# Optimization experiments

Hardware: AMD Instinct MI355X
Metric: run time of the kernel (lower is better)

## Reference

```python
import jax, jax.numpy as jnp
import numpy as np

H, DH = 16, 64  # n_head, head_dim


def setup_inputs() -> dict:
    key = jax.random.key(0)
    ks = jax.random.split(key, 14)
    B, L, D = 2, 1024, 1024
    d = DH

    def lin_w(k, fan_in, shape):
        return jax.random.normal(k, shape, jnp.float32) / np.sqrt(fan_in)

    return {
        "x": jax.random.normal(ks[0], (B, L, D), jnp.float32),
        "Wq": lin_w(ks[1], D, (D, D)),
        "bq": jnp.zeros((D,), jnp.float32),
        "Wk1": lin_w(ks[2], D, (D, D)),
        "bk1": jnp.zeros((D,), jnp.float32),
        "Wk2": lin_w(ks[3], D, (D, D)),
        "bk2": jnp.zeros((D,), jnp.float32),
        "Wg": lin_w(ks[4], d, (d, 1)),
        "bg": jnp.zeros((1,), jnp.float32),
        "Ws": lin_w(ks[5], d, (d, 1)),
        "bs": jnp.zeros((1,), jnp.float32),
        "Wp": lin_w(ks[6], D, (D, D)),
        "bp": jnp.zeros((D,), jnp.float32),
    }


def reference(x, Wq, bq, Wk1, bk1, Wk2, bk2, Wg, bg, Ws, bs, Wp, bp):
    B, L, D = x.shape
    d = DH
    # AR (GLA) branch
    Q = (x @ Wq + bq).reshape(B, L, H, d)
    K = (x @ Wk1 + bk1).reshape(B, L, H, d)
    V = x.reshape(B, L, H, d)
    W = jnp.einsum('blhd,blhe->blhde', K, V)  # (B,L,H,d,d) outer products
    # stable cumprod of sigmoid gate via log-cumsum-exp trick
    G = jax.nn.sigmoid(x.reshape(B, L, H, d) @ Wg + bg)            # (B,L,H,1)
    log_cum = jnp.clip(jnp.cumsum(jnp.log(jnp.clip(G, 1e-6, None)), axis=1), -30.0, 30.0)
    Gc = (jnp.exp(log_cum) + 1e-6)[..., None]                       # (B,L,H,1,1)
    R = jax.nn.silu(K @ Ws + bs)[..., None]                         # (B,L,H,1,1) decay gate
    Wc = jnp.cumsum(W * R / Gc, axis=1) * Gc                        # weighted cumsum
    O1 = jnp.einsum('blhd,blhde->blhe', Q, Wc)                      # (B,L,H,d)
    # MA branch on one-step residuals
    E = V[:, 1:] - O1[:, :-1]                                       # (B,L-1,H,d)
    q2 = -jax.nn.leaky_relu(-Q[:, :-1] / np.sqrt(d), 0.02)          # ma_q_activation (scale head_dim)
    k2 = jax.nn.sigmoid((x[:, :-1] @ Wk2 + bk2) / np.sqrt(D) * 0.02)  # ma_k_activation (scale n_embd)
    k2 = k2.reshape(B, L - 1, H, d)
    W_ma = jnp.cumsum(jnp.einsum('blhd,blhe->blhde', k2, E), axis=1)
    O2 = jnp.einsum('blhd,blhde->blhe', q2, W_ma)
    O2 = jnp.concatenate([jnp.zeros_like(O2[:, :1]), O2], axis=1)   # shift: first MA output is 0
    O = (O1 + O2).reshape(B, L, D)
    return O @ Wp + bp
```

## Files before the change

kernel.cpp:

```cpp
#include <hip/hip_runtime.h>
#include <hip/hip_bf16.h>
#include <math.h>

#define B_  2
#define L_  1024
#define D_  1024
#define H_  16
#define DH_ 64
#define M_  (B_*L_)
#define CHUNK 64
#define NCH (L_/CHUNK)
#define PT 72
#define PS 76

#define KSCALE (0.02f/32.0f)

using bf16x8 = __attribute__((ext_vector_type(8))) short;
using f32x4  = __attribute__((ext_vector_type(4))) float;

__device__ __forceinline__ unsigned short bf16r(float f){
  union{float f; unsigned int u;} x; x.f = f;
  unsigned int r = x.u + 0x7FFF + ((x.u>>16)&1);
  return (unsigned short)(r>>16);
}
__device__ __forceinline__ float bf2f(unsigned short u){
  union{unsigned int u; float f;} x; x.u = ((unsigned int)u)<<16; return x.f;
}

__global__ __launch_bounds__(256) void f32_to_bf16(
  const float* __restrict__ src, unsigned short* __restrict__ dst, int n4)
{
  int i = blockIdx.x*256 + threadIdx.x;
  int stride = gridDim.x*256;
  for (; i < n4; i += stride){
    float4 v = ((const float4*)src)[i];
    ushort4 o;
    o.x = bf16r(v.x); o.y = bf16r(v.y); o.z = bf16r(v.z); o.w = bf16r(v.w);
    ((ushort4*)dst)[i] = o;
  }
}

__global__ __launch_bounds__(256) void convert_wt(
  const float* __restrict__ W0, const float* __restrict__ W1,
  const float* __restrict__ W2, const float* __restrict__ W3,
  unsigned short* __restrict__ T0, unsigned short* __restrict__ T1,
  unsigned short* __restrict__ T2, unsigned short* __restrict__ T3)
{
  int which = blockIdx.z;
  const float* W = which==0?W0: which==1?W1: which==2?W2: W3;
  unsigned short* T = which==0?T0: which==1?T1: which==2?T2: T3;
  __shared__ float tile[64][65];
  int kBase = blockIdx.x*64, nBase = blockIdx.y*64;
  #pragma unroll
  for (int i=0;i<16;i++){
    int idx = threadIdx.x + i*256;
    int r = idx>>6, c = idx&63;
    tile[r][c] = W[(size_t)(kBase+r)*D_ + nBase+c];
  }
  __syncthreads();
  #pragma unroll
  for (int i=0;i<16;i++){
    int idx = threadIdx.x + i*256;
    int n = idx>>6, k = idx&63;
    T[(size_t)(nBase+n)*D_ + kBase+k] = bf16r(tile[k][n]);
  }
}

__device__ __forceinline__ void gemm_core(
    const unsigned short* __restrict__ A, const unsigned short* __restrict__ Bt,
    const float* __restrict__ bias, float* __restrict__ C,
    unsigned short* __restrict__ Cbf, int epi,
    int rowBase, int colBase)
{
  __shared__ __align__(16) unsigned short As[128*32];
  __shared__ __align__(16) unsigned short Bs[64*32];
  int tid = threadIdx.x, w = tid>>6, l = tid&63;
  int lr = l&15, g4 = l>>4;
  f32x4 acc[2][4];
  #pragma unroll
  for (int mi=0;mi<2;mi++)
    #pragma unroll
    for (int ni=0;ni<4;ni++)
      acc[mi][ni] = (f32x4){0.f,0.f,0.f,0.f};

  for (int k0 = 0; k0 < D_; k0 += 32) {
    #pragma unroll
    for (int i=0;i<2;i++){
      int F = (w*2+i)*64 + l;
      int r = F>>2, c16 = F&3;
      int sc = c16 ^ ((r>>1)&3);
      const unsigned short* g = A + (size_t)(rowBase+r)*D_ + k0 + sc*8;
      __builtin_amdgcn_global_load_lds(
        (const __attribute__((address_space(1))) void*)g,
        (__attribute__((address_space(3))) void*)(As + (size_t)(w*2+i)*512), 16, 0, 0);
    }
    {
      int F = w*64 + l;
      int r = F>>2, c16 = F&3;
      int sc = c16 ^ ((r>>1)&3);
      const unsigned short* g = Bt + (size_t)(colBase+r)*D_ + k0 + sc*8;
      __builtin_amdgcn_global_load_lds(
        (const __attribute__((address_space(1))) void*)g,
        (__attribute__((address_space(3))) void*)(Bs + (size_t)w*512), 16, 0, 0);
    }
    __syncthreads();
    bf16x8 af[2], bfr[4];
    #pragma unroll
    for (int mi=0;mi<2;mi++){
      int row = w*32 + mi*16 + lr;
      af[mi] = *(const bf16x8*)(As + row*32 + ((g4 ^ ((row>>1)&3))*8));
    }
    #pragma unroll
    for (int ni=0;ni<4;ni++){
      int n = ni*16 + lr;
      bfr[ni] = *(const bf16x8*)(Bs + n*32 + ((g4 ^ ((n>>1)&3))*8));
    }
    #pragma unroll
    for (int mi=0;mi<2;mi++)
      #pragma unroll
      for (int ni=0;ni<4;ni++)
        acc[mi][ni] = __builtin_amdgcn_mfma_f32_16x16x32_bf16(af[mi], bfr[ni], acc[mi][ni], 0,0,0);
    __syncthreads();
  }

  #pragma unroll
  for (int mi=0;mi<2;mi++){
    #pragma unroll
    for (int ni=0;ni<4;ni++){
      int col = colBase + ni*16 + lr;
      float bv = bias[col];
      #pragma unroll
      for (int r=0;r<4;r++){
        int row = rowBase + w*32 + mi*16 + g4*4 + r;
        float v = acc[mi][ni][r] + bv;
        if (epi) v = 1.f/(1.f + expf(-v*KSCALE));
        C[(size_t)row*D_ + col] = v;
        if (Cbf) Cbf[(size_t)row*D_ + col] = bf16r(v);
      }
    }
  }
}

__global__ __launch_bounds__(256) void gemm3(
  const unsigned short* __restrict__ A,
  const unsigned short* __restrict__ T0, const unsigned short* __restrict__ T1,
  const unsigned short* __restrict__ T2,
  const float* __restrict__ b0, const float* __restrict__ b1, const float* __restrict__ b2,
  float* __restrict__ C0, float* __restrict__ C1, float* __restrict__ C2,
  unsigned short* __restrict__ F0, unsigned short* __restrict__ F1,
  unsigned short* __restrict__ F2)
{
  int z = blockIdx.z;
  const unsigned short* Bt = z==0?T0: z==1?T1: T2;
  const float* bias = z==0?b0: z==1?b1: b2;
  float* C = z==0?C0: z==1?C1: C2;
  unsigned short* F = z==0?F0: z==1?F1: F2;
  gemm_core(A, Bt, bias, C, F, z==2 ? 1 : 0, blockIdx.x*128, blockIdx.y*64);
}

__global__ __launch_bounds__(256) void gemm1(
  const unsigned short* __restrict__ A, const unsigned short* __restrict__ Bt,
  const float* __restrict__ bias, float* __restrict__ C)
{
  gemm_core(A, Bt, bias, C, nullptr, 0, blockIdx.x*128, blockIdx.y*64);
}

__global__ __launch_bounds__(256) void scalars_kernel(
  const float* __restrict__ X, const float* __restrict__ K,
  const float* __restrict__ Wg, const float* __restrict__ bg,
  const float* __restrict__ Ws, const float* __restrict__ bs,
  float* __restrict__ GL, float* __restrict__ RR)
{
  int item = blockIdx.x * 4 + (threadIdx.x >> 6);
  int ln = threadIdx.x & 63;
  int row = item >> 4;
  int h = item & 15;
  float xv = X[(size_t)row*D_ + h*64 + ln];
  float kv = K[(size_t)row*D_ + h*64 + ln];
  float gdot = xv * Wg[ln];
  float rdot = kv * Ws[ln];
  #pragma unroll
  for (int off = 32; off; off >>= 1) {
    gdot += __shfl_xor(gdot, off);
    rdot += __shfl_xor(rdot, off);
  }
  if (ln == 0) {
    float glogit = gdot + bg[0];
    float sg = 1.f/(1.f+expf(-glogit));
    sg = fmaxf(sg, 1e-6f);
    GL[item] = logf(sg);
    float rlogit = rdot + bs[0];
    RR[item] = rlogit / (1.f + expf(-rlogit));
  }
}

__global__ __launch_bounds__(256) void gl_scan(
  const float* __restrict__ GL, const float* __restrict__ RR,
  float* __restrict__ GC, float* __restrict__ CF)
{
  int bh = blockIdx.x * 4 + (threadIdx.x >> 6);
  int b = bh >> 4, h = bh & 15;
  int ln = threadIdx.x & 63;
  float carry = 0.f;
  for (int it = 0; it < 16; ++it) {
    int l = it*64 + ln;
    float x = GL[((size_t)(b*L_ + l))*H_ + h];
    #pragma unroll
    for (int off = 1; off < 64; off <<= 1) {
      float t = __shfl_up(x, off);
      if (ln >= off) x += t;
    }
    float tot = __shfl(x, 63);
    float cum = carry + x;
    carry += tot;
    float lc = fminf(fmaxf(cum, -30.f), 30.f);
    float gc = expf(lc) + 1e-6f;
    GC[(size_t)bh*L_ + l] = gc;
    CF[(size_t)bh*L_ + l] = RR[((size_t)(b*L_ + l))*H_ + h] / gc;
  }
}

__global__ __launch_bounds__(256) void ar_chunk_sum(
  const unsigned short* __restrict__ Kbf, const unsigned short* __restrict__ Xbf,
  const float* __restrict__ CF, float* __restrict__ CS)
{
  int bh = blockIdx.x, c = blockIdx.y;
  int b = bh >> 4, h = bh & 15;
  int row0 = b*L_ + c*CHUNK;
  __shared__ __align__(16) unsigned short kt_t[64*PT];
  __shared__ __align__(16) unsigned short cv_t[64*PT];
  __shared__ __align__(16) float uni[64*PS];
  __shared__ float cf_s[64];
  int tid = threadIdx.x;
  if (tid < 64) cf_s[tid] = CF[(size_t)bh*L_ + c*CHUNK + tid];
  __syncthreads();
  const unsigned short* kg = Kbf + (size_t)row0*D_ + h*64;
  const unsigned short* vg = Xbf + (size_t)row0*D_ + h*64;
  #pragma unroll
  for (int t=0;t<16;t++){
    int idx = tid + t*256;
    int j = idx>>6, d = idx&63;
    kt_t[d*PT + j] = kg[(size_t)j*D_ + d];
    cv_t[d*PT + j] = bf16r(bf2f(vg[(size_t)j*D_ + d]) * cf_s[j]);
  }
  __syncthreads();
  int w = tid>>6, l = tid&63, lr = l&15, g4 = l>>4;
  f32x4 acc[4];
  #pragma unroll
  for (int ni=0;ni<4;ni++) acc[ni] = (f32x4){0.f,0.f,0.f,0.f};
  #pragma unroll
  for (int kk=0;kk<2;kk++){
    bf16x8 a = *(const bf16x8*)&cv_t[(w*16+lr)*PT + kk*32 + g4*8];
    #pragma unroll
    for (int ni=0;ni<4;ni++){
      bf16x8 bb = *(const bf16x8*)&kt_t[(ni*16+lr)*PT + kk*32 + g4*8];
      acc[ni] = __builtin_amdgcn_mfma_f32_16x16x32_bf16(a, bb, acc[ni], 0,0,0);
    }
  }
  #pragma unroll
  for (int ni=0;ni<4;ni++)
    #pragma unroll
    for (int r=0;r<4;r++)
      uni[(w*16+g4*4+r)*PS + ni*16+lr] = acc[ni][r];
  __syncthreads();
  float* out = CS + ((size_t)bh*NCH + c)*4096;
  #pragma unroll
  for (int t=0;t<4;t++){
    int idx = tid + t*256;
    int r = idx>>4, s = idx&15;
    *(float4*)&out[r*64 + s*4] = *(float4*)&uni[r*PS + s*4];
  }
}

__global__ __launch_bounds__(256) void ma_chunk_sum(
  const unsigned short* __restrict__ K2bf, const float* __restrict__ X,
  const float* __restrict__ O1, float* __restrict__ CS)
{
  int bh = blockIdx.x, c = blockIdx.y;
  int b = bh >> 4, h = bh & 15;
  int row0 = b*L_ + c*CHUNK;
  __shared__ __align__(16) unsigned short kt_t[64*PT];
  __shared__ __align__(16) unsigned short et_t[64*PT];
  __shared__ __align__(16) float uni[64*PS];
  int tid = threadIdx.x;
  const unsigned short* kg = K2bf + (size_t)row0*D_ + h*64;
  #pragma unroll
  for (int t=0;t<16;t++){
    int idx = tid + t*256;
    int j = idx>>6, d = idx&63;
    kt_t[d*PT + j] = kg[(size_t)j*D_ + d];
    float ev = 0.f;
    if (c*CHUNK + j < L_-1)
      ev = X[(size_t)(row0+j+1)*D_ + h*64 + d] - O1[(size_t)(row0+j)*D_ + h*64 + d];
    et_t[d*PT + j] = bf16r(ev);
  }
  __syncthreads();
  int w = tid>>6, l = tid&63, lr = l&15, g4 = l>>4;
  f32x4 acc[4];
  #pragma unroll
  for (int ni=0;ni<4;ni++) acc[ni] = (f32x4){0.f,0.f,0.f,0.f};
  #pragma unroll
  for (int kk=0;kk<2;kk++){
    bf16x8 a = *(const bf16x8*)&et_t[(w*16+lr)*PT + kk*32 + g4*8];
    #pragma unroll
    for (int ni=0;ni<4;ni++){
      bf16x8 bb = *(const bf16x8*)&kt_t[(ni*16+lr)*PT + kk*32 + g4*8];
      acc[ni] = __builtin_amdgcn_mfma_f32_16x16x32_bf16(a, bb, acc[ni], 0,0,0);
    }
  }
  #pragma unroll
  for (int ni=0;ni<4;ni++)
    #pragma unroll
    for (int r=0;r<4;r++)
      uni[(w*16+g4*4+r)*PS + ni*16+lr] = acc[ni][r];
  __syncthreads();
  float* out = CS + ((size_t)bh*NCH + c)*4096;
  #pragma unroll
  for (int t=0;t<4;t++){
    int idx = tid + t*256;
    int r = idx>>4, s = idx&15;
    *(float4*)&out[r*64 + s*4] = *(float4*)&uni[r*PS + s*4];
  }
}

__global__ __launch_bounds__(256) void ar_o1_mfma(
  const unsigned short* __restrict__ Qbf, const unsigned short* __restrict__ Kbf,
  const unsigned short* __restrict__ Xbf, const float* __restrict__ CF,
  const float* __restrict__ GC, const float* __restrict__ CS,
  float* __restrict__ O1)
{
  int bh = blockIdx.x, c = blockIdx.y;
  int b = bh >> 4, h = bh & 15;
  int row0 = b*L_ + c*CHUNK;
  __shared__ __align__(16) unsigned short q_t[64*PT];
  __shared__ __align__(16) unsigned short k_t[64*PT];
  __shared__ __align__(16) unsigned short vt_t[64*PT];
  __shared__ __align__(16) unsigned short st_t[64*PT];
  __shared__ __align__(16) float uni[64*PS];
  unsigned short* p_t = (unsigned short*)uni;
  __shared__ float cf_s[64], gc_s[64];
  int tid = threadIdx.x;
  if (tid < 64) {
    cf_s[tid] = CF[(size_t)bh*L_ + c*CHUNK + tid];
    gc_s[tid] = GC[(size_t)bh*L_ + c*CHUNK + tid];
  }
  const unsigned short* qg = Qbf + (size_t)row0*D_ + h*64;
  const unsigned short* kg = Kbf + (size_t)row0*D_ + h*64;
  const unsigned short* vg = Xbf + (size_t)row0*D_ + h*64;
  const float* csb = CS + (size_t)bh*NCH*4096;
  float carry[16];
  #pragma unroll
  for (int i=0;i<16;i++) carry[i] = 0.f;
  for (int c2=0;c2<c;c2++)
    #pragma unroll
    for (int i=0;i<16;i++)
      carry[i] += csb[(size_t)c2*4096 + tid + i*256];
  #pragma unroll
  for (int t=0;t<2;t++){
    int idx = tid + t*256;
    int j = idx>>3, s = idx&7;
    *(uint4*)&q_t[j*PT + s*8] = *(const uint4*)&qg[(size_t)j*D_ + s*8];
    *(uint4*)&k_t[j*PT + s*8] = *(const uint4*)&kg[(size_t)j*D_ + s*8];
  }
  #pragma unroll
  for (int t=0;t<16;t++){
    int idx = tid + t*256;
    int j = idx>>6, d = idx&63;
    vt_t[d*PT + j] = vg[(size_t)j*D_ + d];
  }
  #pragma unroll
  for (int i=0;i<16;i++){
    int idx = tid + i*256;
    st_t[(idx>>6)*PT + (idx&63)] = bf16r(carry[i]);
  }
  __syncthreads();
  int w = tid>>6, l = tid&63, lr = l&15, g4 = l>>4;
  f32x4 acc[4];
  #pragma unroll
  for (int ni=0;ni<4;ni++) acc[ni] = (f32x4){0.f,0.f,0.f,0.f};
  #pragma unroll
  for (int kk=0;kk<2;kk++){
    bf16x8 a = *(const bf16x8*)&q_t[(w*16+lr)*PT + kk*32 + g4*8];
    #pragma unroll
    for (int ni=0;ni<4;ni++){
      bf16x8 bb = *(const bf16x8*)&k_t[(ni*16+lr)*PT + kk*32 + g4*8];
      acc[ni] = __builtin_amdgcn_mfma_f32_16x16x32_bf16(a, bb, acc[ni], 0,0,0);
    }
  }
  #pragma unroll
  for (int ni=0;ni<4;ni++){
    int j = ni*16 + lr;
    float cf = cf_s[j];
    #pragma unroll
    for (int r=0;r<4;r++){
      int row = w*16 + g4*4 + r;
      float v = (j <= row) ? acc[ni][r]*cf : 0.f;
      p_t[row*PT + j] = bf16r(v);
    }
  }
  __syncthreads();
  #pragma unroll
  for (int ni=0;ni<4;ni++) acc[ni] = (f32x4){0.f,0.f,0.f,0.f};
  #pragma unroll
  for (int kk=0;kk<2;kk++){
    bf16x8 ap = *(const bf16x8*)&p_t[(w*16+lr)*PT + kk*32 + g4*8];
    bf16x8 aq = *(const bf16x8*)&q_t[(w*16+lr)*PT + kk*32 + g4*8];
    #pragma unroll
    for (int ni=0;ni<4;ni++){
      bf16x8 bv = *(const bf16x8*)&vt_t[(ni*16+lr)*PT + kk*32 + g4*8];
      bf16x8 bs = *(const bf16x8*)&st_t[(ni*16+lr)*PT + kk*32 + g4*8];
      acc[ni] = __builtin_amdgcn_mfma_f32_16x16x32_bf16(ap, bv, acc[ni], 0,0,0);
      acc[ni] = __builtin_amdgcn_mfma_f32_16x16x32_bf16(aq, bs, acc[ni], 0,0,0);
    }
  }
  __syncthreads();
  #pragma unroll
  for (int ni=0;ni<4;ni++)
    #pragma unroll
    for (int r=0;r<4;r++){
      int row = w*16 + g4*4 + r;
      uni[row*PS + ni*16 + lr] = gc_s[row]*acc[ni][r];
    }
  __syncthreads();
  #pragma unroll
  for (int t=0;t<4;t++){
    int idx = tid + t*256;
    int r = idx>>4, s = idx&15;
    *(float4*)&O1[(size_t)(row0+r)*D_ + h*64 + s*4] = *(float4*)&uni[r*PS + s*4];
  }
}

__global__ __launch_bounds__(256) void ma_o2_mfma(
  const unsigned short* __restrict__ Qbf, const unsigned short* __restrict__ K2bf,
  const float* __restrict__ X, const float* __restrict__ CS,
  const float* __restrict__ O1, unsigned short* __restrict__ Obf)
{
  int bh = blockIdx.x, c = blockIdx.y;
  int b = bh >> 4, h = bh & 15;
  int row0 = b*L_ + c*CHUNK;
  __shared__ __align__(16) unsigned short q_t[64*PT];
  __shared__ __align__(16) unsigned short k_t[64*PT];
  __shared__ __align__(16) unsigned short et_t[64*PT];
  __shared__ __align__(16) unsigned short tt_t[64*PT];
  __shared__ __align__(16) float uni[64*PS];
  unsigned short* p_t = (unsigned short*)uni;
  int tid = threadIdx.x;
  const unsigned short* qg = Qbf  + (size_t)row0*D_ + h*64;
  const unsigned short* kg = K2bf + (size_t)row0*D_ + h*64;
  const float* csb = CS + (size_t)bh*NCH*4096;
  float carry[16];
  #pragma unroll
  for (int i=0;i<16;i++) carry[i] = 0.f;
  for (int c2=0;c2<c;c2++)
    #pragma unroll
    for (int i=0;i<16;i++)
      carry[i] += csb[(size_t)c2*4096 + tid + i*256];
  #pragma unroll
  for (int t=0;t<2;t++){
    int idx = tid + t*256;
    int j = idx>>3, s = idx&7;
    *(uint4*)&k_t[j*PT + s*8] = *(const uint4*)&kg[(size_t)j*D_ + s*8];
  }
  #pragma unroll
  for (int t=0;t<16;t++){
    int idx = tid + t*256;
    int j = idx>>6, d = idx&63;
    float qv = bf2f(qg[(size_t)j*D_ + d]);
    q_t[j*PT + d] = bf16r((qv > 0.f ? 0.02f*qv : qv) * 0.125f);
    float ev = 0.f;
    if (c*CHUNK + j < L_-1)
      ev = X[(size_t)(row0+j+1)*D_ + h*64 + d] - O1[(size_t)(row0+j)*D_ + h*64 + d];
    et_t[d*PT + j] = bf16r(ev);
  }
  #pragma unroll
  for (int i=0;i<16;i++){
    int idx = tid + i*256;
    tt_t[(idx>>6)*PT + (idx&63)] = bf16r(carry[i]);
  }
  __syncthreads();
  int w = tid>>6, l = tid&63, lr = l&15, g4 = l>>4;
  f32x4 acc[4];
  #pragma unroll
  for (int ni=0;ni<4;ni++) acc[ni] = (f32x4){0.f,0.f,0.f,0.f};
  #pragma unroll
  for (int kk=0;kk<2;kk++){
    bf16x8 a = *(const bf16x8*)&q_t[(w*16+lr)*PT + kk*32 + g4*8];
    #pragma unroll
    for (int ni=0;ni<4;ni++){
      bf16x8 bb = *(const bf16x8*)&k_t[(ni*16+lr)*PT + kk*32 + g4*8];
      acc[ni] = __builtin_amdgcn_mfma_f32_16x16x32_bf16(a, bb, acc[ni], 0,0,0);
    }
  }
  #pragma unroll
  for (int ni=0;ni<4;ni++){
    int j = ni*16 + lr;
    #pragma unroll
    for (int r=0;r<4;r++){
      int row = w*16 + g4*4 + r;
      float v = (j <= row) ? acc[ni][r] : 0.f;
      p_t[row*PT + j] = bf16r(v);
    }
  }
  __syncthreads();
  #pragma unroll
  for (int ni=0;ni<4;ni++) acc[ni] = (f32x4){0.f,0.f,0.f,0.f};
  #pragma unroll
  for (int kk=0;kk<2;kk++){
    bf16x8 ap = *(const bf16x8*)&p_t[(w*16+lr)*PT + kk*32 + g4*8];
    bf16x8 aq = *(const bf16x8*)&q_t[(w*16+lr)*PT + kk*32 + g4*8];
    #pragma unroll
    for (int ni=0;ni<4;ni++){
      bf16x8 be = *(const bf16x8*)&et_t[(ni*16+lr)*PT + kk*32 + g4*8];
      bf16x8 bt = *(const bf16x8*)&tt_t[(ni*16+lr)*PT + kk*32 + g4*8];
      acc[ni] = __builtin_amdgcn_mfma_f32_16x16x32_bf16(ap, be, acc[ni], 0,0,0);
      acc[ni] = __builtin_amdgcn_mfma_f32_16x16x32_bf16(aq, bt, acc[ni], 0,0,0);
    }
  }
  __syncthreads();
  #pragma unroll
  for (int ni=0;ni<4;ni++)
    #pragma unroll
    for (int r=0;r<4;r++){
      int row = w*16 + g4*4 + r;
      uni[row*PS + ni*16 + lr] = acc[ni][r];
    }
  __syncthreads();
  #pragma unroll
  for (int t=0;t<4;t++){
    int idx = tid + t*256;
    int r = idx>>4, s = idx&15;
    if (c*CHUNK + r < L_-1) {
      const float4 gv = *(const float4*)&O1[(size_t)(row0+r+1)*D_ + h*64 + s*4];
      float4 uv = *(float4*)&uni[r*PS + s*4];
      ushort4 o;
      o.x = bf16r(gv.x+uv.x); o.y = bf16r(gv.y+uv.y);
      o.z = bf16r(gv.z+uv.z); o.w = bf16r(gv.w+uv.w);
      *(ushort4*)&Obf[(size_t)(row0+r+1)*D_ + h*64 + s*4] = o;
    }
  }
  if (c == 0 && tid < 16) {
    const float4 gv = *(const float4*)&O1[(size_t)row0*D_ + h*64 + tid*4];
    ushort4 o;
    o.x = bf16r(gv.x); o.y = bf16r(gv.y); o.z = bf16r(gv.z); o.w = bf16r(gv.w);
    *(ushort4*)&Obf[(size_t)row0*D_ + h*64 + tid*4] = o;
  }
}

extern "C" void kernel_launch(void* const* d_in, const int* in_sizes, int n_in,
                              void* d_out, int out_size, void* d_ws, size_t ws_size,
                              hipStream_t stream) {
  const float* x  = (const float*)d_in[0];
  const float* Wq = (const float*)d_in[1];
  const float* bq = (const float*)d_in[2];
  const float* Wk1= (const float*)d_in[3];
  const float* bk1= (const float*)d_in[4];
  const float* Wk2= (const float*)d_in[5];
  const float* bk2= (const float*)d_in[6];
  const float* Wg = (const float*)d_in[7];
  const float* bg = (const float*)d_in[8];
  const float* Ws = (const float*)d_in[9];
  const float* bs = (const float*)d_in[10];
  const float* Wp = (const float*)d_in[11];
  const float* bp = (const float*)d_in[12];
  float* out = (float*)d_out;

  float* ws = (float*)d_ws;
  size_t MD = (size_t)M_*D_;
  float* Qb  = ws;
  float* Kb  = Qb  + MD;
  float* K2b = Kb  + MD;
  float* O1b = K2b + MD;
  float* CSb = O1b + MD;
  float* GLb = CSb + (size_t)32*NCH*4096;
  float* RRb = GLb + (size_t)M_*H_;
  float* GCb = RRb + (size_t)M_*H_;
  float* CFb = GCb + (size_t)32*L_;
  unsigned short* Xbf   = (unsigned short*)(CFb + (size_t)32*L_);
  unsigned short* Qbfs  = Xbf  + MD;
  unsigned short* Kbfs  = Qbfs + MD;
  unsigned short* K2bfs = Kbfs + MD;
  unsigned short* Obf   = K2bfs+ MD;
  unsigned short* Wt0   = Obf + MD;
  unsigned short* Wt1   = Wt0 + (size_t)D_*D_;
  unsigned short* Wt2   = Wt1 + (size_t)D_*D_;
  unsigned short* Wt3   = Wt2 + (size_t)D_*D_;

  f32_to_bf16<<<2048, 256, 0, stream>>>(x, Xbf, (int)(MD/4));
  dim3 gt(16, 16, 4);
  convert_wt<<<gt, 256, 0, stream>>>(Wq, Wk1, Wk2, Wp, Wt0, Wt1, Wt2, Wt3);

  dim3 gg(M_/128, D_/64, 3);
  gemm3<<<gg, 256, 0, stream>>>(Xbf, Wt0, Wt1, Wt2, bq, bk1, bk2,
                                Qb, Kb, K2b, Qbfs, Kbfs, K2bfs);

  scalars_kernel<<<(M_*H_)/4, 256, 0, stream>>>(x, Kb, Wg, bg, Ws, bs, GLb, RRb);
  gl_scan<<<8, 256, 0, stream>>>(GLb, RRb, GCb, CFb);

  dim3 gc(32, NCH);
  ar_chunk_sum<<<gc, 256, 0, stream>>>(Kbfs, Xbf, CFb, CSb);
  ar_o1_mfma<<<gc, 256, 0, stream>>>(Qbfs, Kbfs, Xbf, CFb, GCb, CSb, O1b);

  ma_chunk_sum<<<gc, 256, 0, stream>>>(K2bfs, x, O1b, CSb);
  ma_o2_mfma<<<gc, 256, 0, stream>>>(Qbfs, K2bfs, x, CSb, O1b, Obf);

  dim3 go(M_/128, D_/64);
  gemm1<<<go, 256, 0, stream>>>(Obf, Wt3, bp, out);
}
```

Before: 199.6 us.

## Merge conversions, widen QKV GEMM tile, drop fp32 outputs, vectorize chunk loads

Merges the input and weight bf16 conversions into one launch. The three-way projection GEMM moves to 128x128 tiles with direct global-to-LDS loads and now writes only bf16 outputs, removing the fp32 Q/K/K2 stores. The scalar and MA kernels read bf16 K and X instead of fp32. The chunk kernels switch from scalar global reads to 16-byte vector loads, and carry accumulation becomes float4 per thread with a permuted layout. This cuts memory traffic and launch count, but using bf16 X inside the residual and bf16 K for the gate adds rounding error.

```diff
diff --git a/kernel.cpp b/kernel.cpp
--- a/kernel.cpp
+++ b/kernel.cpp
@@ -27,28 +27,32 @@
   union{unsigned int u; float f;} x; x.u = ((unsigned int)u)<<16; return x.f;
 }
 
-__global__ __launch_bounds__(256) void f32_to_bf16(
-  const float* __restrict__ src, unsigned short* __restrict__ dst, int n4)
-{
-  int i = blockIdx.x*256 + threadIdx.x;
-  int stride = gridDim.x*256;
-  for (; i < n4; i += stride){
-    float4 v = ((const float4*)src)[i];
-    ushort4 o;
-    o.x = bf16r(v.x); o.y = bf16r(v.y); o.z = bf16r(v.z); o.w = bf16r(v.w);
-    ((ushort4*)dst)[i] = o;
-  }
-}
-
-__global__ __launch_bounds__(256) void convert_wt(
+__global__ __launch_bounds__(256) void convert_all(
+  const float* __restrict__ X,
   const float* __restrict__ W0, const float* __restrict__ W1,
   const float* __restrict__ W2, const float* __restrict__ W3,
+  unsigned short* __restrict__ Xbf,
   unsigned short* __restrict__ T0, unsigned short* __restrict__ T1,
   unsigned short* __restrict__ T2, unsigned short* __restrict__ T3)
 {
-  int which = blockIdx.z;
-  const float* W = which==0?W0: which==1?W1: which==2?W2: W3;
-  unsigned short* T = which==0?T0: which==1?T1: which==2?T2: T3;
+  int z = blockIdx.z;
+  if (z == 4) {
+    int row = blockIdx.x*64 + (threadIdx.x>>2);
+    int col = blockIdx.y*64 + (threadIdx.x&3)*16;
+    const float4* src = (const float4*)&X[(size_t)row*D_ + col];
+    float4 a=src[0], b=src[1], c=src[2], d=src[3];
+    unsigned short buf[16] = {
+      bf16r(a.x),bf16r(a.y),bf16r(a.z),bf16r(a.w),
+      bf16r(b.x),bf16r(b.y),bf16r(b.z),bf16r(b.w),
+      bf16r(c.x),bf16r(c.y),bf16r(c.z),bf16r(c.w),
+      bf16r(d.x),bf16r(d.y),bf16r(d.z),bf16r(d.w)};
+    *(uint4*)&Xbf[(size_t)row*D_ + col]     = *(uint4*)&buf[0];
+    *(uint4*)&Xbf[(size_t)row*D_ + col + 8] = *(uint4*)&buf[8];
+    return;
+  }
+  if (blockIdx.x >= 16) return;
+  const float* W = z==0?W0: z==1?W1: z==2?W2: W3;
+  unsigned short* T = z==0?T0: z==1?T1: z==2?T2: T3;
   __shared__ float tile[64][65];
   int kBase = blockIdx.x*64, nBase = blockIdx.y*64;
   #pragma unroll
@@ -66,12 +70,90 @@
   }
 }
 
-__device__ __forceinline__ void gemm_core(
-    const unsigned short* __restrict__ A, const unsigned short* __restrict__ Bt,
-    const float* __restrict__ bias, float* __restrict__ C,
-    unsigned short* __restrict__ Cbf, int epi,
-    int rowBase, int colBase)
-{
+__global__ __launch_bounds__(256) void gemm3(
+  const unsigned short* __restrict__ A,
+  const unsigned short* __restrict__ T0, const unsigned short* __restrict__ T1,
+  const unsigned short* __restrict__ T2,
+  const float* __restrict__ b0, const float* __restrict__ b1, const float* __restrict__ b2,
+  unsigned short* __restrict__ F0, unsigned short* __restrict__ F1,
+  unsigned short* __restrict__ F2)
+{
+  int z = blockIdx.z;
+  const unsigned short* Bt = z==0?T0: z==1?T1: T2;
+  const float* bias = z==0?b0: z==1?b1: b2;
+  unsigned short* F = z==0?F0: z==1?F1: F2;
+  int epi = (z==2) ? 1 : 0;
+  int rowBase = blockIdx.x*128, colBase = blockIdx.y*128;
+
+  __shared__ __align__(16) unsigned short As[128*32];
+  __shared__ __align__(16) unsigned short Bs[128*32];
+  int tid = threadIdx.x, w = tid>>6, l = tid&63;
+  int lr = l&15, g4 = l>>4;
+  int wr = w>>1, wc = w&1;
+  f32x4 acc[4][4];
+  #pragma unroll
+  for (int mi=0;mi<4;mi++)
+    #pragma unroll
+    for (int ni=0;ni<4;ni++)
+      acc[mi][ni] = (f32x4){0.f,0.f,0.f,0.f};
+
+  for (int k0 = 0; k0 < D_; k0 += 32) {
+    #pragma unroll
+    for (int i=0;i<2;i++){
+      int Fi = (w*2+i)*64 + l;
+      int r = Fi>>2, c16 = Fi&3;
+      int sc = c16 ^ ((r>>1)&3);
+      const unsigned short* ga = A  + (size_t)(rowBase+r)*D_ + k0 + sc*8;
+      const unsigned short* gb = Bt + (size_t)(colBase+r)*D_ + k0 + sc*8;
+      __builtin_amdgcn_global_load_lds(
+        (const __attribute__((address_space(1))) void*)ga,
+        (__attribute__((address_space(3))) void*)(As + (size_t)(w*2+i)*512), 16, 0, 0);
+      __builtin_amdgcn_global_load_lds(
+        (const __attribute__((address_space(1))) void*)gb,
+        (__attribute__((address_space(3))) void*)(Bs + (size_t)(w*2+i)*512), 16, 0, 0);
+    }
+    __syncthreads();
+    bf16x8 af[4], bfr[4];
+    #pragma unroll
+    for (int mi=0;mi<4;mi++){
+      int row = wr*64 + mi*16 + lr;
+      af[mi] = *(const bf16x8*)(As + row*32 + ((g4 ^ ((row>>1)&3))*8));
+    }
+    #pragma unroll
+    for (int ni=0;ni<4;ni++){
+      int n = wc*64 + ni*16 + lr;
+      bfr[ni] = *(const bf16x8*)(Bs + n*32 + ((g4 ^ ((n>>1)&3))*8));
+    }
+    #pragma unroll
+    for (int mi=0;mi<4;mi++)
+      #pragma unroll
+      for (int ni=0;ni<4;ni++)
+        acc[mi][ni] = __builtin_amdgcn_mfma_f32_16x16x32_bf16(af[mi], bfr[ni], acc[mi][ni], 0,0,0);
+    __syncthreads();
+  }
+
+  #pragma unroll
+  for (int mi=0;mi<4;mi++){
+    #pragma unroll
+    for (int ni=0;ni<4;ni++){
+      int col = colBase + wc*64 + ni*16 + lr;
+      float bv = bias[col];
+      #pragma unroll
+      for (int r=0;r<4;r++){
+        int row = rowBase + wr*64 + mi*16 + g4*4 + r;
+        float v = acc[mi][ni][r] + bv;
+        if (epi) v = 1.f/(1.f + expf(-v*KSCALE));
+        F[(size_t)row*D_ + col] = bf16r(v);
+      }
+    }
+  }
+}
+
+__global__ __launch_bounds__(256) void gemm1(
+  const unsigned short* __restrict__ A, const unsigned short* __restrict__ Bt,
+  const float* __restrict__ bias, float* __restrict__ C)
+{
+  int rowBase = blockIdx.x*128, colBase = blockIdx.y*64;
   __shared__ __align__(16) unsigned short As[128*32];
   __shared__ __align__(16) unsigned short Bs[64*32];
   int tid = threadIdx.x, w = tid>>6, l = tid&63;
@@ -132,41 +214,14 @@
       #pragma unroll
       for (int r=0;r<4;r++){
         int row = rowBase + w*32 + mi*16 + g4*4 + r;
-        float v = acc[mi][ni][r] + bv;
-        if (epi) v = 1.f/(1.f + expf(-v*KSCALE));
-        C[(size_t)row*D_ + col] = v;
-        if (Cbf) Cbf[(size_t)row*D_ + col] = bf16r(v);
+        C[(size_t)row*D_ + col] = acc[mi][ni][r] + bv;
       }
     }
   }
 }
 
-__global__ __launch_bounds__(256) void gemm3(
-  const unsigned short* __restrict__ A,
-  const unsigned short* __restrict__ T0, const unsigned short* __restrict__ T1,
-  const unsigned short* __restrict__ T2,
-  const float* __restrict__ b0, const float* __restrict__ b1, const float* __restrict__ b2,
-  float* __restrict__ C0, float* __restrict__ C1, float* __restrict__ C2,
-  unsigned short* __restrict__ F0, unsigned short* __restrict__ F1,
-  unsigned short* __restrict__ F2)
-{
-  int z = blockIdx.z;
-  const unsigned short* Bt = z==0?T0: z==1?T1: T2;
-  const float* bias = z==0?b0: z==1?b1: b2;
-  float* C = z==0?C0: z==1?C1: C2;
-  unsigned short* F = z==0?F0: z==1?F1: F2;
-  gemm_core(A, Bt, bias, C, F, z==2 ? 1 : 0, blockIdx.x*128, blockIdx.y*64);
-}
-
-__global__ __launch_bounds__(256) void gemm1(
-  const unsigned short* __restrict__ A, const unsigned short* __restrict__ Bt,
-  const float* __restrict__ bias, float* __restrict__ C)
-{
-  gemm_core(A, Bt, bias, C, nullptr, 0, blockIdx.x*128, blockIdx.y*64);
-}
-
 __global__ __launch_bounds__(256) void scalars_kernel(
-  const float* __restrict__ X, const float* __restrict__ K,
+  const float* __restrict__ X, const unsigned short* __restrict__ Kbf,
   const float* __restrict__ Wg, const float* __restrict__ bg,
   const float* __restrict__ Ws, const float* __restrict__ bs,
   float* __restrict__ GL, float* __restrict__ RR)
@@ -176,7 +231,7 @@
   int row = item >> 4;
   int h = item & 15;
   float xv = X[(size_t)row*D_ + h*64 + ln];
-  float kv = K[(size_t)row*D_ + h*64 + ln];
+  float kv = bf2f(Kbf[(size_t)row*D_ + h*64 + ln]);
   float gdot = xv * Wg[ln];
   float rdot = kv * Ws[ln];
   #pragma unroll
@@ -237,11 +292,17 @@
   const unsigned short* kg = Kbf + (size_t)row0*D_ + h*64;
   const unsigned short* vg = Xbf + (size_t)row0*D_ + h*64;
   #pragma unroll
-  for (int t=0;t<16;t++){
-    int idx = tid + t*256;
-    int j = idx>>6, d = idx&63;
-    kt_t[d*PT + j] = kg[(size_t)j*D_ + d];
-    cv_t[d*PT + j] = bf16r(bf2f(vg[(size_t)j*D_ + d]) * cf_s[j]);
+  for (int t=0;t<2;t++){
+    int j = (tid>>3) + t*32;
+    int d0 = (tid&7)*8;
+    bf16x8 kv = *(const bf16x8*)&kg[(size_t)j*D_ + d0];
+    bf16x8 vv = *(const bf16x8*)&vg[(size_t)j*D_ + d0];
+    float cfj = cf_s[j];
+    #pragma unroll
+    for (int i=0;i<8;i++){
+      kt_t[(d0+i)*PT + j] = (unsigned short)kv[i];
+      cv_t[(d0+i)*PT + j] = bf16r(bf2f((unsigned short)vv[i]) * cfj);
+    }
   }
   __syncthreads();
   int w = tid>>6, l = tid&63, lr = l&15, g4 = l>>4;
@@ -273,7 +334,7 @@
 }
 
 __global__ __launch_bounds__(256) void ma_chunk_sum(
-  const unsigned short* __restrict__ K2bf, const float* __restrict__ X,
+  const unsigned short* __restrict__ K2bf, const unsigned short* __restrict__ Xbf,
   const float* __restrict__ O1, float* __restrict__ CS)
 {
   int bh = blockIdx.x, c = blockIdx.y;
@@ -285,14 +346,25 @@
   int tid = threadIdx.x;
   const unsigned short* kg = K2bf + (size_t)row0*D_ + h*64;
   #pragma unroll
-  for (int t=0;t<16;t++){
-    int idx = tid + t*256;
-    int j = idx>>6, d = idx&63;
-    kt_t[d*PT + j] = kg[(size_t)j*D_ + d];
-    float ev = 0.f;
-    if (c*CHUNK + j < L_-1)
-      ev = X[(size_t)(row0+j+1)*D_ + h*64 + d] - O1[(size_t)(row0+j)*D_ + h*64 + d];
-    et_t[d*PT + j] = bf16r(ev);
+  for (int t=0;t<2;t++){
+    int j = (tid>>3) + t*32;
+    int e0 = (tid&7)*8;
+    bf16x8 kv = *(const bf16x8*)&kg[(size_t)j*D_ + e0];
+    float ev[8] = {0.f,0.f,0.f,0.f,0.f,0.f,0.f,0.f};
+    if (c*CHUNK + j < L_-1){
+      bf16x8 xv = *(const bf16x8*)&Xbf[(size_t)(row0+j+1)*D_ + h*64 + e0];
+      const float4* op = (const float4*)&O1[(size_t)(row0+j)*D_ + h*64 + e0];
+      float4 o0 = op[0], o1v = op[1];
+      ev[0]=bf2f((unsigned short)xv[0])-o0.x;  ev[1]=bf2f((unsigned short)xv[1])-o0.y;
+      ev[2]=bf2f((unsigned short)xv[2])-o0.z;  ev[3]=bf2f((unsigned short)xv[3])-o0.w;
+      ev[4]=bf2f((unsigned short)xv[4])-o1v.x; ev[5]=bf2f((unsigned short)xv[5])-o1v.y;
+      ev[6]=bf2f((unsigned short)xv[6])-o1v.z; ev[7]=bf2f((unsigned short)xv[7])-o1v.w;
+    }
+    #pragma unroll
+    for (int i=0;i<8;i++){
+      kt_t[(e0+i)*PT + j] = (unsigned short)kv[i];
+      et_t[(e0+i)*PT + j] = bf16r(ev[i]);
+    }
   }
   __syncthreads();
   int w = tid>>6, l = tid&63, lr = l&15, g4 = l>>4;
@@ -348,13 +420,26 @@
   const unsigned short* kg = Kbf + (size_t)row0*D_ + h*64;
   const unsigned short* vg = Xbf + (size_t)row0*D_ + h*64;
   const float* csb = CS + (size_t)bh*NCH*4096;
-  float carry[16];
-  #pragma unroll
-  for (int i=0;i<16;i++) carry[i] = 0.f;
-  for (int c2=0;c2<c;c2++)
-    #pragma unroll
-    for (int i=0;i<16;i++)
-      carry[i] += csb[(size_t)c2*4096 + tid + i*256];
+  {
+    float carry[16];
+    #pragma unroll
+    for (int i=0;i<16;i++) carry[i] = 0.f;
+    const float* cb = csb + (size_t)tid*16;
+    for (int c2=0;c2<c;c2++){
+      const float4* p4 = (const float4*)(cb + (size_t)c2*4096);
+      float4 a0=p4[0],a1=p4[1],a2=p4[2],a3=p4[3];
+      carry[0]+=a0.x; carry[1]+=a0.y; carry[2]+=a0.z; carry[3]+=a0.w;
+      carry[4]+=a1.x; carry[5]+=a1.y; carry[6]+=a1.z; carry[7]+=a1.w;
+      carry[8]+=a2.x; carry[9]+=a2.y; carry[10]+=a2.z; carry[11]+=a2.w;
+      carry[12]+=a3.x; carry[13]+=a3.y; carry[14]+=a3.z; carry[15]+=a3.w;
+    }
+    unsigned short buf[16];
+    #pragma unroll
+    for (int i=0;i<16;i++) buf[i] = bf16r(carry[i]);
+    int row = tid>>2, col = (tid&3)*16;
+    *(uint4*)&st_t[row*PT + col]     = *(uint4*)&buf[0];
+    *(uint4*)&st_t[row*PT + col + 8] = *(uint4*)&buf[8];
+  }
   #pragma unroll
   for (int t=0;t<2;t++){
     int idx = tid + t*256;
@@ -363,15 +448,12 @@
     *(uint4*)&k_t[j*PT + s*8] = *(const uint4*)&kg[(size_t)j*D_ + s*8];
   }
   #pragma unroll
-  for (int t=0;t<16;t++){
-    int idx = tid + t*256;
-    int j = idx>>6, d = idx&63;
-    vt_t[d*PT + j] = vg[(size_t)j*D_ + d];
-  }
-  #pragma unroll
-  for (int i=0;i<16;i++){
-    int idx = tid + i*256;
-    st_t[(idx>>6)*PT + (idx&63)] = bf16r(carry[i]);
+  for (int t=0;t<2;t++){
+    int j = (tid>>3) + t*32;
+    int e0 = (tid&7)*8;
+    bf16x8 vv = *(const bf16x8*)&vg[(size_t)j*D_ + e0];
+    #pragma unroll
+    for (int i=0;i<8;i++) vt_t[(e0+i)*PT + j] = (unsigned short)vv[i];
   }
   __syncthreads();
   int w = tid>>6, l = tid&63, lr = l&15, g4 = l>>4;
@@ -432,7 +514,7 @@
 
 __global__ __launch_bounds__(256) void ma_o2_mfma(
   const unsigned short* __restrict__ Qbf, const unsigned short* __restrict__ K2bf,
-  const float* __restrict__ X, const float* __restrict__ CS,
+  const unsigned short* __restrict__ Xbf, const float* __restrict__ CS,
   const float* __restrict__ O1, unsigned short* __restrict__ Obf)
 {
   int bh = blockIdx.x, c = blockIdx.y;
@@ -448,13 +530,26 @@
   const unsigned short* qg = Qbf  + (size_t)row0*D_ + h*64;
   const unsigned short* kg = K2bf + (size_t)row0*D_ + h*64;
   const float* csb = CS + (size_t)bh*NCH*4096;
-  float carry[16];
-  #pragma unroll
-  for (int i=0;i<16;i++) carry[i] = 0.f;
-  for (int c2=0;c2<c;c2++)
-    #pragma unroll
-    for (int i=0;i<16;i++)
-      carry[i] += csb[(size_t)c2*4096 + tid + i*256];
+  {
+    float carry[16];
+    #pragma unroll
+    for (int i=0;i<16;i++) carry[i] = 0.f;
+    const float* cb = csb + (size_t)tid*16;
+    for (int c2=0;c2<c;c2++){
+      const float4* p4 = (const float4*)(cb + (size_t)c2*4096);
+      float4 a0=p4[0],a1=p4[1],a2=p4[2],a3=p4[3];
+      carry[0]+=a0.x; carry[1]+=a0.y; carry[2]+=a0.z; carry[3]+=a0.w;
+      carry[4]+=a1.x; carry[5]+=a1.y; carry[6]+=a1.z; carry[7]+=a1.w;
+      carry[8]+=a2.x; carry[9]+=a2.y; carry[10]+=a2.z; carry[11]+=a2.w;
+      carry[12]+=a3.x; carry[13]+=a3.y; carry[14]+=a3.z; carry[15]+=a3.w;
+    }
+    unsigned short buf[16];
+    #pragma unroll
+    for (int i=0;i<16;i++) buf[i] = bf16r(carry[i]);
+    int row = tid>>2, col = (tid&3)*16;
+    *(uint4*)&tt_t[row*PT + col]     = *(uint4*)&buf[0];
+    *(uint4*)&tt_t[row*PT + col + 8] = *(uint4*)&buf[8];
+  }
   #pragma unroll
   for (int t=0;t<2;t++){
     int idx = tid + t*256;
@@ -462,20 +557,29 @@
     *(uint4*)&k_t[j*PT + s*8] = *(const uint4*)&kg[(size_t)j*D_ + s*8];
   }
   #pragma unroll
-  for (int t=0;t<16;t++){
-    int idx = tid + t*256;
-    int j = idx>>6, d = idx&63;
-    float qv = bf2f(qg[(size_t)j*D_ + d]);
-    q_t[j*PT + d] = bf16r((qv > 0.f ? 0.02f*qv : qv) * 0.125f);
-    float ev = 0.f;
-    if (c*CHUNK + j < L_-1)
-      ev = X[(size_t)(row0+j+1)*D_ + h*64 + d] - O1[(size_t)(row0+j)*D_ + h*64 + d];
-    et_t[d*PT + j] = bf16r(ev);
-  }
-  #pragma unroll
-  for (int i=0;i<16;i++){
-    int idx = tid + i*256;
-    tt_t[(idx>>6)*PT + (idx&63)] = bf16r(carry[i]);
+  for (int t=0;t<2;t++){
+    int j = (tid>>3) + t*32;
+    int d0 = (tid&7)*8;
+    bf16x8 qv = *(const bf16x8*)&qg[(size_t)j*D_ + d0];
+    unsigned short qb[8];
+    #pragma unroll
+    for (int i=0;i<8;i++){
+      float q = bf2f((unsigned short)qv[i]);
+      qb[i] = bf16r((q > 0.f ? 0.02f*q : q) * 0.125f);
+    }
+    *(uint4*)&q_t[j*PT + d0] = *(uint4*)&qb[0];
+    float ev[8] = {0.f,0.f,0.f,0.f,0.f,0.f,0.f,0.f};
+    if (c*CHUNK + j < L_-1){
+      bf16x8 xv = *(const bf16x8*)&Xbf[(size_t)(row0+j+1)*D_ + h*64 + d0];
+      const float4* op = (const float4*)&O1[(size_t)(row0+j)*D_ + h*64 + d0];
+      float4 o0 = op[0], o1v = op[1];
+      ev[0]=bf2f((unsigned short)xv[0])-o0.x;  ev[1]=bf2f((unsigned short)xv[1])-o0.y;
+      ev[2]=bf2f((unsigned short)xv[2])-o0.z;  ev[3]=bf2f((unsigned short)xv[3])-o0.w;
+      ev[4]=bf2f((unsigned short)xv[4])-o1v.x; ev[5]=bf2f((unsigned short)xv[5])-o1v.y;
+      ev[6]=bf2f((unsigned short)xv[6])-o1v.z; ev[7]=bf2f((unsigned short)xv[7])-o1v.w;
+    }
+    #pragma unroll
+    for (int i=0;i<8;i++) et_t[(d0+i)*PT + j] = bf16r(ev[i]);
   }
   __syncthreads();
   int w = tid>>6, l = tid&63, lr = l&15, g4 = l>>4;
@@ -566,10 +670,7 @@
 
   float* ws = (float*)d_ws;
   size_t MD = (size_t)M_*D_;
-  float* Qb  = ws;
-  float* Kb  = Qb  + MD;
-  float* K2b = Kb  + MD;
-  float* O1b = K2b + MD;
+  float* O1b = ws;
   float* CSb = O1b + MD;
   float* GLb = CSb + (size_t)32*NCH*4096;
   float* RRb = GLb + (size_t)M_*H_;
@@ -585,23 +686,21 @@
   unsigned short* Wt2   = Wt1 + (size_t)D_*D_;
   unsigned short* Wt3   = Wt2 + (size_t)D_*D_;
 
-  f32_to_bf16<<<2048, 256, 0, stream>>>(x, Xbf, (int)(MD/4));
-  dim3 gt(16, 16, 4);
-  convert_wt<<<gt, 256, 0, stream>>>(Wq, Wk1, Wk2, Wp, Wt0, Wt1, Wt2, Wt3);
-
-  dim3 gg(M_/128, D_/64, 3);
-  gemm3<<<gg, 256, 0, stream>>>(Xbf, Wt0, Wt1, Wt2, bq, bk1, bk2,
-                                Qb, Kb, K2b, Qbfs, Kbfs, K2bfs);
-
-  scalars_kernel<<<(M_*H_)/4, 256, 0, stream>>>(x, Kb, Wg, bg, Ws, bs, GLb, RRb);
+  dim3 gcv(32, 16, 5);
+  convert_all<<<gcv, 256, 0, stream>>>(x, Wq, Wk1, Wk2, Wp, Xbf, Wt0, Wt1, Wt2, Wt3);
+
+  dim3 gg(M_/128, D_/128, 3);
+  gemm3<<<gg, 256, 0, stream>>>(Xbf, Wt0, Wt1, Wt2, bq, bk1, bk2, Qbfs, Kbfs, K2bfs);
+
+  scalars_kernel<<<(M_*H_)/4, 256, 0, stream>>>(x, Kbfs, Wg, bg, Ws, bs, GLb, RRb);
   gl_scan<<<8, 256, 0, stream>>>(GLb, RRb, GCb, CFb);
 
   dim3 gc(32, NCH);
   ar_chunk_sum<<<gc, 256, 0, stream>>>(Kbfs, Xbf, CFb, CSb);
   ar_o1_mfma<<<gc, 256, 0, stream>>>(Qbfs, Kbfs, Xbf, CFb, GCb, CSb, O1b);
 
-  ma_chunk_sum<<<gc, 256, 0, stream>>>(K2bfs, x, O1b, CSb);
-  ma_o2_mfma<<<gc, 256, 0, stream>>>(Qbfs, K2bfs, x, CSb, O1b, Obf);
+  ma_chunk_sum<<<gc, 256, 0, stream>>>(K2bfs, Xbf, O1b, CSb);
+  ma_o2_mfma<<<gc, 256, 0, stream>>>(Qbfs, K2bfs, Xbf, CSb, O1b, Obf);
 
   dim3 go(M_/128, D_/64);
   gemm1<<<go, 256, 0, stream>>>(Obf, Wt3, bp, out);
```

Result: faster. 184.7 us (-7.5%).
